# Kernel optimization log

Measured on AMD Instinct MI355X. Metric: run time of the kernel, lower is better.

The kernel has to match this reference:

```python
import jax, jax.numpy as jnp
import numpy as np

DIM = 128
NUM_LAYERS = 2
FF_MULT = 4
RADIUS = 0.2
K = 8
B, N, L = 8, 2048, 4096
NEG = -1e30


def setup_inputs() -> dict:
    key = jax.random.key(0)
    ks = jax.random.split(key, 12)
    C = DIM
    s = 1.0 / np.sqrt(C)
    w = lambda k, shape, sc: jax.random.normal(k, shape, dtype=jnp.float32) * sc
    inp = {
        "q_xyz": jax.random.uniform(ks[0], (B, N, 3), dtype=jnp.float32),
        "q_feat": jax.random.normal(ks[1], (B, N, C), dtype=jnp.float32),
        "kv_xyz": jax.random.uniform(ks[2], (B, L, 3), dtype=jnp.float32),
        "kv_feat": jax.random.normal(ks[3], (B, L, C), dtype=jnp.float32),
        "kv_pad": jnp.zeros((B, L), dtype=bool),
        # PointTransformerConv params (stacked over layers)
        "W_lin": w(ks[4], (NUM_LAYERS, C, C), s),   # value projection (with bias)
        "b_lin": jnp.zeros((NUM_LAYERS, C), jnp.float32),
        "W_src": w(ks[5], (NUM_LAYERS, C, C), s),   # lin_src, no bias
        "W_dst": w(ks[6], (NUM_LAYERS, C, C), s),   # lin_dst, no bias
        "W_attn": w(ks[7], (NUM_LAYERS, C, C), s),  # attn_nn = Linear+ReLU
        "b_attn": jnp.zeros((NUM_LAYERS, C), jnp.float32),
        "ln1_g": jnp.ones((NUM_LAYERS, C), jnp.float32),
        "ln1_b": jnp.zeros((NUM_LAYERS, C), jnp.float32),
        "W_ff1": w(ks[8], (NUM_LAYERS, C, FF_MULT * C), s),
        "b_ff1": jnp.zeros((NUM_LAYERS, FF_MULT * C), jnp.float32),
        "W_ff2": w(ks[9], (NUM_LAYERS, FF_MULT * C, C), 1.0 / np.sqrt(FF_MULT * C)),
        "b_ff2": jnp.zeros((NUM_LAYERS, C), jnp.float32),
        "ln2_g": jnp.ones((NUM_LAYERS, C), jnp.float32),
        "ln2_b": jnp.zeros((NUM_LAYERS, C), jnp.float32),
    }
    return inp


def _layernorm(x, g, b):
    mu = x.mean(-1, keepdims=True)
    var = ((x - mu) ** 2).mean(-1, keepdims=True)
    return (x - mu) * jax.lax.rsqrt(var + 1e-5) * g + b


def _gather(feats, idx):
    # feats: [B, L, C], idx: [B, N, K] -> [B, N, K, C]
    b, n, k = idx.shape
    g = jnp.take_along_axis(feats, idx.reshape(b, n * k)[:, :, None], axis=1)
    return g.reshape(b, n, k, feats.shape[-1])


def _forward(q_xyz, q_feat, kv_xyz, kv_feat, kv_pad,
             W_lin, b_lin, W_src, W_dst, W_attn, b_attn,
             ln1_g, ln1_b, W_ff1, b_ff1, W_ff2, b_ff2, ln2_g, ln2_b):
    # radius neighbor search (per-batch, fixed K neighbors with validity mask)
    d2 = jnp.sum((q_xyz[:, :, None, :] - kv_xyz[:, None, :, :]) ** 2, axis=-1)  # [B,N,L]
    valid_pair = (d2 <= RADIUS * RADIUS) & (~kv_pad)[:, None, :]
    negd = jnp.where(valid_pair, -d2, NEG)
    negv, idx = jax.lax.top_k(negd, K)          # [B,N,K] nearest-in-ball
    evalid = negv > 0.5 * NEG                   # edge validity mask [B,N,K]

    out = q_feat
    for i in range(NUM_LAYERS):
        # PointTransformerConv, pos_nn = ZeroPos => delta = 0
        aj = _gather(kv_feat @ W_src[i], idx)                    # [B,N,K,C]
        vj = _gather(kv_feat @ W_lin[i] + b_lin[i], idx)         # [B,N,K,C]
        ai = out @ W_dst[i]                                      # [B,N,C]
        logits = jax.nn.relu((ai[:, :, None, :] - aj) @ W_attn[i] + b_attn[i])
        logits = jnp.where(evalid[..., None], logits, NEG)
        m = logits.max(axis=2, keepdims=True)
        e = jnp.exp(logits - m) * evalid[..., None]
        attn = e / jnp.maximum(e.sum(axis=2, keepdims=True), 1e-9)  # per-channel softmax over neighbors
        upd = jnp.sum(attn * vj, axis=2)                         # [B,N,C] scatter-add over edges
        out = _layernorm(out + upd, ln1_g[i], ln1_b[i])
        h = jax.nn.gelu(out @ W_ff1[i] + b_ff1[i], approximate=False)
        out = _layernorm(out + h @ W_ff2[i] + b_ff2[i], ln2_g[i], ln2_b[i])
    return out


def reference(q_xyz, q_feat, kv_xyz, kv_feat, kv_pad,
              W_lin, b_lin, W_src, W_dst, W_attn, b_attn,
              ln1_g, ln1_b, W_ff1, b_ff1, W_ff2, b_ff2, ln2_g, ln2_b):
    return _forward(q_xyz, q_feat, kv_xyz, kv_feat, kv_pad,
                    W_lin, b_lin, W_src, W_dst, W_attn, b_attn,
                    ln1_g, ln1_b, W_ff1, b_ff1, W_ff2, b_ff2, ln2_g, ln2_b)
```

## Files before the change

kernel.cpp:

```cpp
#include <hip/hip_runtime.h>
#include <hip/hip_bf16.h>
#include <math.h>

#define DIM 128
#define BB 8
#define NN 2048
#define LL 4096
#define KK 8

typedef __hip_bfloat16 bf16;
typedef unsigned long long ull;
typedef __attribute__((ext_vector_type(8))) short short8;
typedef __attribute__((ext_vector_type(4))) float float4v;

__device__ __forceinline__ float toF(float x){ return x; }
__device__ __forceinline__ float toF(bf16 x){ return __bfloat162float(x); }
__device__ __forceinline__ void st(float* p, float v){ *p = v; }
__device__ __forceinline__ void st(bf16*  p, float v){ *p = __float2bfloat16(v); }
__device__ __forceinline__ unsigned short f2bf(float f){
  union { bf16 b; unsigned short u; } cv; cv.b = __float2bfloat16(f); return cv.u;
}

__device__ __forceinline__ float gelu_exact(float x){
  return 0.5f * x * (1.0f + erff(x * 0.70710678118654752f));
}

__device__ __forceinline__ float waveSum64(float v){
  #pragma unroll
  for (int o = 32; o > 0; o >>= 1) v += __shfl_xor(v, o, 64);
  return v;
}
__device__ __forceinline__ float quadSum16(float v){
  #pragma unroll
  for (int o = 8; o > 0; o >>= 1) v += __shfl_xor(v, o, 64);
  return v;
}

__device__ __forceinline__ void topk_insert_u(ull (&m)[KK], ull key){
  m[KK-1] = key;
  #pragma unroll
  for (int t = KK-1; t > 0; --t){
    if (m[t] < m[t-1]){ ull tmp = m[t]; m[t] = m[t-1]; m[t-1] = tmp; }
  }
}

#define NC3 125
__global__ __launch_bounds__(1024) void knn_bin(const float* __restrict__ kv_xyz,
                                                const float* __restrict__ q_xyz,
                                                float4* __restrict__ bpts,
                                                int* __restrict__ offs ,
                                                int* __restrict__ qsrt )
{
  __shared__ int cnt[NC3];
  __shared__ int off[NC3+1];
  const int b   = blockIdx.x & 7;
  const int role= blockIdx.x >> 3;
  const int tid = threadIdx.x;
  if (tid < NC3) cnt[tid] = 0;
  __syncthreads();
  if (role == 0){
    const float* kvp = kv_xyz + (size_t)b * LL * 3;
    float px[4], py[4], pz[4]; int pc[4];
    #pragma unroll
    for (int i = 0; i < 4; i++){
      const int e = tid + i*1024;
      px[i] = kvp[3*e]; py[i] = kvp[3*e+1]; pz[i] = kvp[3*e+2];
      const int cx = min((int)(px[i]*5.f), 4);
      const int cy = min((int)(py[i]*5.f), 4);
      const int cz = min((int)(pz[i]*5.f), 4);
      pc[i] = (cz*5 + cy)*5 + cx;
      atomicAdd(&cnt[pc[i]], 1);
    }
    __syncthreads();
    if (tid == 0){
      int acc = 0;
      for (int c = 0; c < NC3; c++){ off[c] = acc; acc += cnt[c]; }
      off[NC3] = acc;
    }
    __syncthreads();
    if (tid < NC3) cnt[tid] = 0;
    __syncthreads();
    float4* dst = bpts + (size_t)b * LL;
    #pragma unroll
    for (int i = 0; i < 4; i++){
      const int e = tid + i*1024;
      const int pos = off[pc[i]] + atomicAdd(&cnt[pc[i]], 1);
      dst[pos] = make_float4(px[i], py[i], pz[i], __int_as_float(e));
    }
    if (tid < NC3 + 1) offs[b*126 + tid] = off[tid];
  } else {
    const float* qp = q_xyz + (size_t)b * NN * 3;
    int pc[2];
    #pragma unroll
    for (int i = 0; i < 2; i++){
      const int e = tid + i*1024;
      const float x = qp[3*e], y = qp[3*e+1], z = qp[3*e+2];
      const int cx = min((int)(x*5.f), 4);
      const int cy = min((int)(y*5.f), 4);
      const int cz = min((int)(z*5.f), 4);
      pc[i] = (cz*5 + cy)*5 + cx;
      atomicAdd(&cnt[pc[i]], 1);
    }
    __syncthreads();
    if (tid == 0){
      int acc = 0;
      for (int c = 0; c < NC3; c++){ off[c] = acc; acc += cnt[c]; }
      off[NC3] = acc;
    }
    __syncthreads();
    if (tid < NC3) cnt[tid] = 0;
    __syncthreads();
    int* dst = qsrt + (size_t)b * NN;
    #pragma unroll
    for (int i = 0; i < 2; i++){
      const int e = tid + i*1024;
      const int pos = off[pc[i]] + atomicAdd(&cnt[pc[i]], 1);
      dst[pos] = e;
    }
  }
}

#define QBLK 8
#define SPL 32
__global__ __launch_bounds__(256) void knn_query(const float* __restrict__ q_xyz,
                                                 const float4* __restrict__ bpts,
                                                 const int* __restrict__ offs,
                                                 const int* __restrict__ qsrt,
                                                 int* __restrict__ idx)
{
  __shared__ ull cd[QBLK*257];
  const int tid  = threadIdx.x;
  const int s    = tid >> 3;
  const int qloc = tid & 7;
  const int b    = blockIdx.y;
  const int qbase = blockIdx.x * QBLK;
  const int qid = qsrt[b*NN + qbase + qloc];
  const size_t qo = ((size_t)b * NN + qid) * 3;
  const float qx = q_xyz[qo], qy = q_xyz[qo+1], qz = q_xyz[qo+2];
  const ull THRKEY = ((ull)0x3D23D70Bu << 32);
  ull kthr = THRKEY;
  ull m[KK];
  #pragma unroll
  for (int k = 0; k < KK; k++) m[k] = ~0ULL;
  const int qcx = min((int)(qx*5.f), 4);
  const int qcy = min((int)(qy*5.f), 4);
  const int qcz = min((int)(qz*5.f), 4);
  const int* ofb = offs + b*126;
  const float4* bp = bpts + (size_t)b * LL;
  const int cx0 = max(qcx-1, 0), cx1 = min(qcx+1, 4);
  for (int cz = max(qcz-1,0); cz <= min(qcz+1,4); cz++){
    for (int cy = max(qcy-1,0); cy <= min(qcy+1,4); cy++){
      const int rowc = (cz*5 + cy)*5;
      const int pstart = ofb[rowc + cx0];
      const int pend   = ofb[rowc + cx1 + 1];
      for (int p = pstart + s; p < pend; p += SPL){
        const float4 pt = bp[p];
        const float dx = qx - pt.x, dy = qy - pt.y, dz = qz - pt.z;
        const float d2 = dx*dx + dy*dy + dz*dz;
        const ull key = ((ull)__float_as_uint(d2) << 32) | (unsigned)__float_as_int(pt.w);
        if (key < kthr){
          topk_insert_u(m, key);
          kthr = (m[KK-1] < THRKEY) ? m[KK-1] : THRKEY;
        }
      }
    }
  }
  #pragma unroll
  for (int k = 0; k < KK; k++) cd[qloc*257 + s*8 + k] = m[k];
  __syncthreads();
  if (tid < 64){
    const int q = tid >> 3, g = tid & 7;
    ull mm[KK];
    #pragma unroll
    for (int k = 0; k < KK; k++) mm[k] = ~0ULL;
    #pragma unroll
    for (int u = 0; u < 4; u++){
      const int sl = g + 8*u;
      #pragma unroll
      for (int k = 0; k < KK; k++){
        const ull key = cd[q*257 + sl*8 + k];
        if (key < mm[KK-1]) topk_insert_u(mm, key);
      }
    }
    #pragma unroll
    for (int k = 0; k < KK; k++) cd[q*257 + g*8 + k] = mm[k];
    if (tid < QBLK){
      ull f[KK];
      #pragma unroll
      for (int k = 0; k < KK; k++) f[k] = ~0ULL;
      for (int j = 0; j < 64; j++){
        const ull key = cd[tid*257 + j];
        if (key < f[KK-1]) topk_insert_u(f, key);
      }
      const int oq = b * NN + qsrt[b*NN + qbase + tid];
      #pragma unroll
      for (int k = 0; k < KK; k++) idx[oq*KK + k] = (int)(unsigned)(f[k] & 0xFFFFFFFFu);
    }
  }
}

__device__ __forceinline__ void packOne(const float* __restrict__ src,
                                        bf16* __restrict__ dst, int idx, int nshift){
  const int k = idx >> nshift;
  const int n = idx & ((1 << nshift) - 1);
  const int N = 1 << nshift;
  st(&dst[((size_t)(k>>3)*N + n)*8 + (k&7)], src[idx]);
}

__global__ __launch_bounds__(256) void prep_weights(const float* __restrict__ Wlin,
                                                    const float* __restrict__ Wff1,
                                                    const float* __restrict__ Wff2,
                                                    const float* __restrict__ Wsrc,
                                                    const float* __restrict__ Wdst,
                                                    const float* __restrict__ Wattn,
                                                    bf16* __restrict__ WlinP,
                                                    bf16* __restrict__ Wff1P,
                                                    bf16* __restrict__ Wff2P,
                                                    bf16* __restrict__ WsaP,
                                                    bf16* __restrict__ WdaP)
{
  __shared__ float row[2][DIM];
  const int bid = blockIdx.x;
  if (bid < 1152){
    int i = bid*256 + threadIdx.x;
    if (i < 32768){
      const int l = i >> 14, r = i & 16383;
      packOne(Wlin + (size_t)l*16384, WlinP + (size_t)l*16384, r, 7);
    } else if (i < 163840){
      i -= 32768;
      const int l = i >> 16, r = i & 65535;
      packOne(Wff1 + (size_t)l*65536, Wff1P + (size_t)l*65536, r, 9);
    } else if (i < 294912){
      i -= 163840;
      const int l = i >> 16, r = i & 65535;
      packOne(Wff2 + (size_t)l*65536, Wff2P + (size_t)l*65536, r, 7);
    }
  } else {
    const int half = threadIdx.x >> 7;
    const int c = threadIdx.x & 127;
    const int tt = (bid - 1152)*2 + half;
    const int r = tt & 127, which = (tt >> 7) & 1, lay = tt >> 8;
    const float* Wx = (which ? Wdst : Wsrc) + (size_t)lay*DIM*DIM;
    const float* Wa = Wattn + (size_t)lay*DIM*DIM;
    row[half][c] = Wx[r*DIM + c];
    __syncthreads();
    float acc = 0.f;
    for (int j = 0; j < DIM; j++) acc = fmaf(row[half][j], Wa[j*DIM + c], acc);
    bf16* dst = (which ? WdaP : WsaP) + (size_t)lay*DIM*DIM;
    st(&dst[((size_t)(r>>3)*DIM + c)*8 + (r&7)], acc);
  }
}

__device__ __forceinline__ void stage_A_f32(const float* __restrict__ A, size_t r0,
                                            int kd, int kc, unsigned short* As, int tid){
  #pragma unroll
  for (int i = 0; i < 8; i++){
    const int f = tid + i*256;
    const int row = f >> 5, c4 = (f & 31) * 4;
    const float4 v = *(const float4*)&A[(r0+row)*kd + kc + c4];
    uint2 u;
    u.x = (unsigned)f2bf(v.x) | ((unsigned)f2bf(v.y) << 16);
    u.y = (unsigned)f2bf(v.z) | ((unsigned)f2bf(v.w) << 16);
    *(uint2*)&As[row*136 + c4] = u;
  }
}
__device__ __forceinline__ void stage_A_bf16(const bf16* __restrict__ A, size_t r0,
                                             int kd, int kc, unsigned short* As, int tid){
  #pragma unroll
  for (int i = 0; i < 8; i++){
    const int f = tid + i*256;
    const int row = f >> 5, c4 = (f & 31) * 4;
    *(uint2*)&As[row*136 + c4] = *(const uint2*)&A[(r0+row)*kd + kc + c4];
  }
}

template<typename TA, int NDIM, bool GELU>
__global__ __launch_bounds__(256) void mfma_single(const TA* __restrict__ A,
                                                   const bf16* __restrict__ Wp,
                                                   const float* __restrict__ bias,
                                                   bf16* __restrict__ Y)
{
  __shared__ __align__(16) unsigned short As[64*136];
  const int tid = threadIdx.x;
  const size_t r0 = (size_t)blockIdx.x * 64;
  const int nblk = blockIdx.y * 128;
  if (sizeof(TA) == 4) stage_A_f32((const float*)A, r0, 128, 0, As, tid);
  else                 stage_A_bf16((const bf16*)A, r0, 128, 0, As, tid);
  __syncthreads();
  const int wid = tid >> 6, ln = tid & 63, qd = ln >> 4, cl = ln & 15;
  float4v acc[8];
  #pragma unroll
  for (int t = 0; t < 8; t++) acc[t] = (float4v){0.f,0.f,0.f,0.f};
  #pragma unroll
  for (int ks = 0; ks < 4; ks++){
    const short8 a = *(const short8*)&As[(wid*16 + cl)*136 + (ks*4 + qd)*8];
    const short8* wb = (const short8*)Wp + (size_t)(ks*4 + qd)*NDIM + nblk + cl;
    #pragma unroll
    for (int t = 0; t < 8; t++){
      const short8 b = wb[t*16];
      acc[t] = __builtin_amdgcn_mfma_f32_16x16x32_bf16(a, b, acc[t], 0, 0, 0);
    }
  }
  #pragma unroll
  for (int t = 0; t < 8; t++){
    const int col = nblk + t*16 + cl;
    const float bv = bias ? bias[col] : 0.f;
    #pragma unroll
    for (int r = 0; r < 4; r++){
      const size_t row = r0 + wid*16 + qd*4 + r;
      float v = acc[t][r] + bv;
      if (GELU) v = gelu_exact(v);
      st(&Y[row*NDIM + col], v);
    }
  }
}

__global__ __launch_bounds__(256) void mfma_dual_qa(const float* __restrict__ kvf,
                                                    const float* __restrict__ featIn,
                                                    const bf16* __restrict__ Wp0,
                                                    const bf16* __restrict__ Wp1,
                                                    const bf16* __restrict__ WpQ,
                                                    const float* __restrict__ bias1,
                                                    bf16* __restrict__ Y0,
                                                    bf16* __restrict__ Y1,
                                                    bf16* __restrict__ Yq)
{
  __shared__ __align__(16) unsigned short As[64*136];
  const int tid = threadIdx.x;
  const int wid = tid >> 6, ln = tid & 63, qd = ln >> 4, cl = ln & 15;
  if (blockIdx.x < 512){
    const size_t r0 = (size_t)blockIdx.x * 64;
    stage_A_f32(kvf, r0, 128, 0, As, tid);
    __syncthreads();
    float4v ac0[8], ac1[8];
    #pragma unroll
    for (int t = 0; t < 8; t++){ ac0[t] = (float4v){0.f,0.f,0.f,0.f}; ac1[t] = (float4v){0.f,0.f,0.f,0.f}; }
    #pragma unroll
    for (int ks = 0; ks < 4; ks++){
      const short8 a = *(const short8*)&As[(wid*16 + cl)*136 + (ks*4 + qd)*8];
      const size_t wo = (size_t)(ks*4 + qd)*DIM + cl;
      const short8* wb0 = (const short8*)Wp0 + wo;
      const short8* wb1 = (const short8*)Wp1 + wo;
      #pragma unroll
      for (int t = 0; t < 8; t++){
        const short8 b0 = wb0[t*16];
        ac0[t] = __builtin_amdgcn_mfma_f32_16x16x32_bf16(a, b0, ac0[t], 0, 0, 0);
        const short8 b1 = wb1[t*16];
        ac1[t] = __builtin_amdgcn_mfma_f32_16x16x32_bf16(a, b1, ac1[t], 0, 0, 0);
      }
    }
    #pragma unroll
    for (int t = 0; t < 8; t++){
      const int col = t*16 + cl;
      const float bv = bias1[col];
      #pragma unroll
      for (int r = 0; r < 4; r++){
        const size_t row = r0 + wid*16 + qd*4 + r;
        st(&Y0[row*DIM + col], ac0[t][r]);
        st(&Y1[row*DIM + col], ac1[t][r] + bv);
      }
    }
  } else {
    const size_t r0 = (size_t)(blockIdx.x - 512) * 64;
    stage_A_f32(featIn, r0, 128, 0, As, tid);
    __syncthreads();
    float4v acc[8];
    #pragma unroll
    for (int t = 0; t < 8; t++) acc[t] = (float4v){0.f,0.f,0.f,0.f};
    #pragma unroll
    for (int ks = 0; ks < 4; ks++){
      const short8 a = *(const short8*)&As[(wid*16 + cl)*136 + (ks*4 + qd)*8];
      const short8* wb = (const short8*)WpQ + (size_t)(ks*4 + qd)*DIM + cl;
      #pragma unroll
      for (int t = 0; t < 8; t++){
        const short8 b = wb[t*16];
        acc[t] = __builtin_amdgcn_mfma_f32_16x16x32_bf16(a, b, acc[t], 0, 0, 0);
      }
    }
    #pragma unroll
    for (int t = 0; t < 8; t++){
      const int col = t*16 + cl;
      #pragma unroll
      for (int r = 0; r < 4; r++){
        const size_t row = r0 + wid*16 + qd*4 + r;
        st(&Yq[row*DIM + col], acc[t][r]);
      }
    }
  }
}

__global__ __launch_bounds__(256) void mfma_ff2ln(const bf16* __restrict__ A,
                                                  const bf16* __restrict__ Wp,
                                                  const float* __restrict__ b2,
                                                  const bf16* __restrict__ resid,
                                                  const float* __restrict__ g,
                                                  const float* __restrict__ bb,
                                                  float* __restrict__ Y)
{
  __shared__ __align__(16) unsigned short As[64*136];
  const int tid = threadIdx.x;
  const size_t r0 = (size_t)blockIdx.x * 64;
  const int wid = tid >> 6, ln = tid & 63, qd = ln >> 4, cl = ln & 15;
  float4v acc[8];
  #pragma unroll
  for (int t = 0; t < 8; t++) acc[t] = (float4v){0.f,0.f,0.f,0.f};
  for (int kc = 0; kc < 512; kc += 128){
    __syncthreads();
    stage_A_bf16(A, r0, 512, kc, As, tid);
    __syncthreads();
    const int k8c = kc >> 3;
    #pragma unroll
    for (int ks = 0; ks < 4; ks++){
      const short8 a = *(const short8*)&As[(wid*16 + cl)*136 + (ks*4 + qd)*8];
      const short8* wb = (const short8*)Wp + (size_t)(k8c + ks*4 + qd)*DIM + cl;
      #pragma unroll
      for (int t = 0; t < 8; t++){
        const short8 b = wb[t*16];
        acc[t] = __builtin_amdgcn_mfma_f32_16x16x32_bf16(a, b, acc[t], 0, 0, 0);
      }
    }
  }
  float v[8][4];
  #pragma unroll
  for (int t = 0; t < 8; t++){
    const int col = t*16 + cl;
    const float bv = b2[col];
    #pragma unroll
    for (int r = 0; r < 4; r++){
      const size_t row = r0 + wid*16 + qd*4 + r;
      v[t][r] = acc[t][r] + bv + toF(resid[row*DIM + col]);
    }
  }
  #pragma unroll
  for (int r = 0; r < 4; r++){
    float s = 0.f;
    #pragma unroll
    for (int t = 0; t < 8; t++) s += v[t][r];
    const float mu = quadSum16(s) * (1.f/DIM);
    float q = 0.f;
    #pragma unroll
    for (int t = 0; t < 8; t++){ const float d = v[t][r] - mu; q += d*d; }
    const float inv = rsqrtf(quadSum16(q) * (1.f/DIM) + 1e-5f);
    const size_t row = r0 + wid*16 + qd*4 + r;
    #pragma unroll
    for (int t = 0; t < 8; t++){
      const int col = t*16 + cl;
      Y[row*DIM + col] = (v[t][r] - mu) * inv * g[col] + bb[col];
    }
  }
}

__global__ __launch_bounds__(256) void attn_ln1(const bf16* __restrict__ qA,
                                                const bf16* __restrict__ srcA,
                                                const bf16* __restrict__ linp,
                                                const int* __restrict__ idx,
                                                const int* __restrict__ qsrt,
                                                const float* __restrict__ b_attn,
                                                const float* __restrict__ feat,
                                                const float* __restrict__ g,
                                                const float* __restrict__ bb,
                                                bf16* __restrict__ out1)
{
  const int tid = threadIdx.x;
  const int wv = tid >> 6, ln = tid & 63;
  const int sp = blockIdx.x * 4 + wv;
  const int b = sp >> 11;
  const int q = b * NN + qsrt[b*NN + (sp & 2047)];
  const bf16* sbase = srcA + (size_t)b * LL * DIM;
  const bf16* vbase = linp + (size_t)b * LL * DIM;
  const int c0 = ln, c1 = ln + 64;
  const float qa0 = toF(qA[(size_t)q*DIM + c0]) + b_attn[c0];
  const float qa1 = toF(qA[(size_t)q*DIM + c1]) + b_attn[c1];
  int ids[KK]; float l0[KK], l1[KK];
  float m0 = -1e30f, m1 = -1e30f;
  #pragma unroll
  for (int k = 0; k < KK; k++){
    const int id = idx[q*KK + k]; ids[k] = id;
    if (id >= 0){
      const float s0 = toF(sbase[(size_t)id*DIM + c0]);
      const float s1 = toF(sbase[(size_t)id*DIM + c1]);
      l0[k] = fmaxf(qa0 - s0, 0.f); m0 = fmaxf(m0, l0[k]);
      l1[k] = fmaxf(qa1 - s1, 0.f); m1 = fmaxf(m1, l1[k]);
    } else { l0[k] = 0.f; l1[k] = 0.f; }
  }
  float sum0 = 0.f, sum1 = 0.f, upd0 = 0.f, upd1 = 0.f;
  #pragma unroll
  for (int k = 0; k < KK; k++) if (ids[k] >= 0){
    const float e0 = expf(l0[k] - m0); l0[k] = e0; sum0 += e0;
    const float e1 = expf(l1[k] - m1); l1[k] = e1; sum1 += e1;
  }
  if (sum0 > 0.f){
    const float i0 = 1.f / sum0, i1 = 1.f / sum1;
    #pragma unroll
    for (int k = 0; k < KK; k++) if (ids[k] >= 0){
      upd0 = fmaf(l0[k]*i0, toF(vbase[(size_t)ids[k]*DIM + c0]), upd0);
      upd1 = fmaf(l1[k]*i1, toF(vbase[(size_t)ids[k]*DIM + c1]), upd1);
    }
  }
  const float x0 = feat[(size_t)q*DIM + c0] + upd0;
  const float x1 = feat[(size_t)q*DIM + c1] + upd1;
  const float mu = waveSum64(x0 + x1) * (1.f/DIM);
  const float d0 = x0 - mu, d1 = x1 - mu;
  const float var = waveSum64(d0*d0 + d1*d1) * (1.f/DIM);
  const float inv = rsqrtf(var + 1e-5f);
  st(&out1[(size_t)q*DIM + c0], d0 * inv * g[c0] + bb[c0]);
  st(&out1[(size_t)q*DIM + c1], d1 * inv * g[c1] + bb[c1]);
}

extern "C" void kernel_launch(void* const* d_in, const int* in_sizes, int n_in,
                              void* d_out, int out_size, void* d_ws, size_t ws_size,
                              hipStream_t stream)
{
  const float* q_xyz  = (const float*)d_in[0];
  const float* q_feat = (const float*)d_in[1];
  const float* kv_xyz = (const float*)d_in[2];
  const float* kv_feat= (const float*)d_in[3];
  const float* W_lin  = (const float*)d_in[5];
  const float* b_lin  = (const float*)d_in[6];
  const float* W_src  = (const float*)d_in[7];
  const float* W_dst  = (const float*)d_in[8];
  const float* W_attn = (const float*)d_in[9];
  const float* b_attn = (const float*)d_in[10];
  const float* ln1_g  = (const float*)d_in[11];
  const float* ln1_b  = (const float*)d_in[12];
  const float* W_ff1  = (const float*)d_in[13];
  const float* b_ff1  = (const float*)d_in[14];
  const float* W_ff2  = (const float*)d_in[15];
  const float* b_ff2  = (const float*)d_in[16];
  const float* ln2_g  = (const float*)d_in[17];
  const float* ln2_b  = (const float*)d_in[18];
  float* out = (float*)d_out;

  const int MQ  = BB * NN;
  const int MKV = BB * LL;

  char* p = (char*)d_ws;
  int*    idxb  = (int*)p;    p += (size_t)MQ * KK * 4;
  float4* bpts  = (float4*)p; p += (size_t)BB * LL * 16;
  int*    boffs = (int*)p;    p += (size_t)BB * 126 * 4;
  int*    qsrt  = (int*)p;    p += (size_t)BB * NN * 4;
  bf16*  WsaP  = (bf16*)p;  p += (size_t)2 * DIM * DIM * 2;
  bf16*  WdaP  = (bf16*)p;  p += (size_t)2 * DIM * DIM * 2;
  bf16*  WlinP = (bf16*)p;  p += (size_t)2 * DIM * DIM * 2;
  bf16*  Wff1P = (bf16*)p;  p += (size_t)2 * DIM * 4*DIM * 2;
  bf16*  Wff2P = (bf16*)p;  p += (size_t)2 * 4*DIM * DIM * 2;
  float* feat  = (float*)p; p += (size_t)MQ * DIM * 4;
  bf16*  out1  = (bf16*)p;  p += (size_t)MQ * DIM * 2;
  bf16*  srcA  = (bf16*)p;  p += (size_t)MKV * DIM * 2;
  bf16*  linp  = (bf16*)p;  p += (size_t)MKV * DIM * 2;
  bf16*  qA    = (bf16*)p;  p += (size_t)MQ * DIM * 2;
  bf16*  hbuf  = srcA;

  knn_bin<<<16, 1024, 0, stream>>>(kv_xyz, q_xyz, bpts, boffs, qsrt);
  knn_query<<<dim3(NN/QBLK, BB), 256, 0, stream>>>(q_xyz, bpts, boffs, qsrt, idxb);
  prep_weights<<<1152 + 256, 256, 0, stream>>>(W_lin, W_ff1, W_ff2, W_src, W_dst,
                                               W_attn, WlinP, Wff1P, Wff2P, WsaP, WdaP);

  for (int i = 0; i < 2; i++){
    const size_t w128 = (size_t)i * DIM * DIM;
    const size_t w512 = (size_t)i * DIM * 4*DIM;
    const float* featIn = (i == 0) ? q_feat : feat;

    mfma_dual_qa<<<MKV/64 + MQ/64, 256, 0, stream>>>(kv_feat, featIn,
        WsaP + w128, WlinP + w128, WdaP + w128, b_lin + i*DIM, srcA, linp, qA);
    attn_ln1<<<MQ/4, 256, 0, stream>>>(qA, srcA, linp, idxb, qsrt, b_attn + i*DIM,
                                       featIn, ln1_g + i*DIM, ln1_b + i*DIM, out1);
    mfma_single<bf16, 512, true><<<dim3(MQ/64, 4), 256, 0, stream>>>(
        out1, Wff1P + w512, b_ff1 + i*4*DIM, hbuf);
    float* ydst = (i == 1) ? out : feat;
    mfma_ff2ln<<<MQ/64, 256, 0, stream>>>(hbuf, Wff2P + w512, b_ff2 + i*DIM, out1,
                                          ln2_g + i*DIM, ln2_b + i*DIM, ydst);
  }
}
```

Before: 297.4 us.

## Merge binning and weight prep kernels, remap kNN lanes, vectorize attention loads

```diff
diff --git a/kernel.cpp b/kernel.cpp
--- a/kernel.cpp
+++ b/kernel.cpp
@@ -20,6 +20,13 @@
 __device__ __forceinline__ unsigned short f2bf(float f){
   union { bf16 b; unsigned short u; } cv; cv.b = __float2bfloat16(f); return cv.u;
 }
+__device__ __forceinline__ float2 ld2bf(const bf16* p){
+  const unsigned u = *(const unsigned*)p;
+  return make_float2(__uint_as_float(u << 16), __uint_as_float(u & 0xFFFF0000u));
+}
+__device__ __forceinline__ void st2bf(bf16* p, float a, float b){
+  *(unsigned*)p = (unsigned)f2bf(a) | ((unsigned)f2bf(b) << 16);
+}
 
 __device__ __forceinline__ float gelu_exact(float x){
   return 0.5f * x * (1.0f + erff(x * 0.70710678118654752f));
@@ -45,78 +52,128 @@
 }
 
 #define NC3 125
-__global__ __launch_bounds__(1024) void knn_bin(const float* __restrict__ kv_xyz,
-                                                const float* __restrict__ q_xyz,
-                                                float4* __restrict__ bpts,
-                                                int* __restrict__ offs ,
-                                                int* __restrict__ qsrt )
+__device__ __forceinline__ void packOne(const float* __restrict__ src,
+                                        bf16* __restrict__ dst, int idx, int nshift){
+  const int k = idx >> nshift;
+  const int n = idx & ((1 << nshift) - 1);
+  const int N = 1 << nshift;
+  st(&dst[((size_t)(k>>3)*N + n)*8 + (k&7)], src[idx]);
+}
+
+__global__ __launch_bounds__(1024) void setup_all(const float* __restrict__ kv_xyz,
+                                                  const float* __restrict__ q_xyz,
+                                                  float4* __restrict__ bpts,
+                                                  int* __restrict__ offs,
+                                                  int* __restrict__ qsrt,
+                                                  const float* __restrict__ Wlin,
+                                                  const float* __restrict__ Wff1,
+                                                  const float* __restrict__ Wff2,
+                                                  const float* __restrict__ Wsrc,
+                                                  const float* __restrict__ Wdst,
+                                                  const float* __restrict__ Wattn,
+                                                  bf16* __restrict__ WlinP,
+                                                  bf16* __restrict__ Wff1P,
+                                                  bf16* __restrict__ Wff2P,
+                                                  bf16* __restrict__ WsaP,
+                                                  bf16* __restrict__ WdaP)
 {
   __shared__ int cnt[NC3];
   __shared__ int off[NC3+1];
-  const int b   = blockIdx.x & 7;
-  const int role= blockIdx.x >> 3;
+  __shared__ float row[8][DIM];
+  const int bid = blockIdx.x;
   const int tid = threadIdx.x;
-  if (tid < NC3) cnt[tid] = 0;
-  __syncthreads();
-  if (role == 0){
-    const float* kvp = kv_xyz + (size_t)b * LL * 3;
-    float px[4], py[4], pz[4]; int pc[4];
-    #pragma unroll
-    for (int i = 0; i < 4; i++){
-      const int e = tid + i*1024;
-      px[i] = kvp[3*e]; py[i] = kvp[3*e+1]; pz[i] = kvp[3*e+2];
-      const int cx = min((int)(px[i]*5.f), 4);
-      const int cy = min((int)(py[i]*5.f), 4);
-      const int cz = min((int)(pz[i]*5.f), 4);
-      pc[i] = (cz*5 + cy)*5 + cx;
-      atomicAdd(&cnt[pc[i]], 1);
-    }
-    __syncthreads();
-    if (tid == 0){
-      int acc = 0;
-      for (int c = 0; c < NC3; c++){ off[c] = acc; acc += cnt[c]; }
-      off[NC3] = acc;
-    }
-    __syncthreads();
+  if (bid < 16){
+    const int b   = bid & 7;
+    const int role= bid >> 3;
     if (tid < NC3) cnt[tid] = 0;
     __syncthreads();
-    float4* dst = bpts + (size_t)b * LL;
-    #pragma unroll
-    for (int i = 0; i < 4; i++){
-      const int e = tid + i*1024;
-      const int pos = off[pc[i]] + atomicAdd(&cnt[pc[i]], 1);
-      dst[pos] = make_float4(px[i], py[i], pz[i], __int_as_float(e));
-    }
-    if (tid < NC3 + 1) offs[b*126 + tid] = off[tid];
+    if (role == 0){
+      const float* kvp = kv_xyz + (size_t)b * LL * 3;
+      float px[4], py[4], pz[4]; int pc[4];
+      #pragma unroll
+      for (int i = 0; i < 4; i++){
+        const int e = tid + i*1024;
+        px[i] = kvp[3*e]; py[i] = kvp[3*e+1]; pz[i] = kvp[3*e+2];
+        const int cx = min((int)(px[i]*5.f), 4);
+        const int cy = min((int)(py[i]*5.f), 4);
+        const int cz = min((int)(pz[i]*5.f), 4);
+        pc[i] = (cz*5 + cy)*5 + cx;
+        atomicAdd(&cnt[pc[i]], 1);
+      }
+      __syncthreads();
+      if (tid == 0){
+        int acc = 0;
+        for (int c = 0; c < NC3; c++){ off[c] = acc; acc += cnt[c]; }
+        off[NC3] = acc;
+      }
+      __syncthreads();
+      if (tid < NC3) cnt[tid] = 0;
+      __syncthreads();
+      float4* dst = bpts + (size_t)b * LL;
+      #pragma unroll
+      for (int i = 0; i < 4; i++){
+        const int e = tid + i*1024;
+        const int pos = off[pc[i]] + atomicAdd(&cnt[pc[i]], 1);
+        dst[pos] = make_float4(px[i], py[i], pz[i], __int_as_float(e));
+      }
+      if (tid < NC3 + 1) offs[b*126 + tid] = off[tid];
+    } else {
+      const float* qp = q_xyz + (size_t)b * NN * 3;
+      int pc[2];
+      #pragma unroll
+      for (int i = 0; i < 2; i++){
+        const int e = tid + i*1024;
+        const float x = qp[3*e], y = qp[3*e+1], z = qp[3*e+2];
+        const int cx = min((int)(x*5.f), 4);
+        const int cy = min((int)(y*5.f), 4);
+        const int cz = min((int)(z*5.f), 4);
+        pc[i] = (cz*5 + cy)*5 + cx;
+        atomicAdd(&cnt[pc[i]], 1);
+      }
+      __syncthreads();
+      if (tid == 0){
+        int acc = 0;
+        for (int c = 0; c < NC3; c++){ off[c] = acc; acc += cnt[c]; }
+        off[NC3] = acc;
+      }
+      __syncthreads();
+      if (tid < NC3) cnt[tid] = 0;
+      __syncthreads();
+      int* dst = qsrt + (size_t)b * NN;
+      #pragma unroll
+      for (int i = 0; i < 2; i++){
+        const int e = tid + i*1024;
+        const int pos = off[pc[i]] + atomicAdd(&cnt[pc[i]], 1);
+        dst[pos] = e;
+      }
+    }
+  } else if (bid < 304){
+    int i = (bid - 16)*1024 + tid;
+    if (i < 32768){
+      const int l = i >> 14, r = i & 16383;
+      packOne(Wlin + (size_t)l*16384, WlinP + (size_t)l*16384, r, 7);
+    } else if (i < 163840){
+      i -= 32768;
+      const int l = i >> 16, r = i & 65535;
+      packOne(Wff1 + (size_t)l*65536, Wff1P + (size_t)l*65536, r, 9);
+    } else {
+      i -= 163840;
+      const int l = i >> 16, r = i & 65535;
+      packOne(Wff2 + (size_t)l*65536, Wff2P + (size_t)l*65536, r, 7);
+    }
   } else {
-    const float* qp = q_xyz + (size_t)b * NN * 3;
-    int pc[2];
-    #pragma unroll
-    for (int i = 0; i < 2; i++){
-      const int e = tid + i*1024;
-      const float x = qp[3*e], y = qp[3*e+1], z = qp[3*e+2];
-      const int cx = min((int)(x*5.f), 4);
-      const int cy = min((int)(y*5.f), 4);
-      const int cz = min((int)(z*5.f), 4);
-      pc[i] = (cz*5 + cy)*5 + cx;
-      atomicAdd(&cnt[pc[i]], 1);
-    }
+    const int grp = tid >> 7;
+    const int c = tid & 127;
+    const int tt = (bid - 304)*8 + grp;
+    const int r = tt & 127, which = (tt >> 7) & 1, lay = tt >> 8;
+    const float* Wx = (which ? Wdst : Wsrc) + (size_t)lay*DIM*DIM;
+    const float* Wa = Wattn + (size_t)lay*DIM*DIM;
+    row[grp][c] = Wx[r*DIM + c];
     __syncthreads();
-    if (tid == 0){
-      int acc = 0;
-      for (int c = 0; c < NC3; c++){ off[c] = acc; acc += cnt[c]; }
-      off[NC3] = acc;
-    }
-    __syncthreads();
-    if (tid < NC3) cnt[tid] = 0;
-    __syncthreads();
-    int* dst = qsrt + (size_t)b * NN;
-    #pragma unroll
-    for (int i = 0; i < 2; i++){
-      const int e = tid + i*1024;
-      const int pos = off[pc[i]] + atomicAdd(&cnt[pc[i]], 1);
-      dst[pos] = e;
-    }
+    float acc = 0.f;
+    for (int j = 0; j < DIM; j++) acc = fmaf(row[grp][j], Wa[j*DIM + c], acc);
+    bf16* dst = (which ? WdaP : WsaP) + (size_t)lay*DIM*DIM;
+    st(&dst[((size_t)(r>>3)*DIM + c)*8 + (r&7)], acc);
   }
 }
 
@@ -130,8 +187,8 @@
 {
   __shared__ ull cd[QBLK*257];
   const int tid  = threadIdx.x;
-  const int s    = tid >> 3;
-  const int qloc = tid & 7;
+  const int s    = tid & 31;
+  const int qloc = tid >> 5;
   const int b    = blockIdx.y;
   const int qbase = blockIdx.x * QBLK;
   const int qid = qsrt[b*NN + qbase + qloc];
@@ -151,22 +208,30 @@
   for (int cz = max(qcz-1,0); cz <= min(qcz+1,4); cz++){
     for (int cy = max(qcy-1,0); cy <= min(qcy+1,4); cy++){
       const int rowc = (cz*5 + cy)*5;
-      const int pstart = ofb[rowc + cx0];
-      const int pend   = ofb[rowc + cx1 + 1];
-      for (int p = pstart + s; p < pend; p += SPL){
-        const float4 pt = bp[p];
-        const float dx = qx - pt.x, dy = qy - pt.y, dz = qz - pt.z;
-        const float d2 = dx*dx + dy*dy + dz*dz;
-        const ull key = ((ull)__float_as_uint(d2) << 32) | (unsigned)__float_as_int(pt.w);
-        if (key < kthr){
-          topk_insert_u(m, key);
-          kthr = (m[KK-1] < THRKEY) ? m[KK-1] : THRKEY;
+      const int pend = ofb[rowc + cx1 + 1];
+      int p = ofb[rowc + cx0] + s;
+      if (p < pend){
+        float4 pt = bp[p];
+        while (true){
+          const int pn = p + SPL;
+          const bool hn = pn < pend;
+          float4 nx;
+          if (hn) nx = bp[pn];
+          const float dx = qx - pt.x, dy = qy - pt.y, dz = qz - pt.z;
+          const float d2 = dx*dx + dy*dy + dz*dz;
+          const ull key = ((ull)__float_as_uint(d2) << 32) | (unsigned)__float_as_int(pt.w);
+          if (key < kthr){
+            topk_insert_u(m, key);
+            kthr = (m[KK-1] < THRKEY) ? m[KK-1] : THRKEY;
+          }
+          if (!hn) break;
+          pt = nx; p = pn;
         }
       }
     }
   }
   #pragma unroll
-  for (int k = 0; k < KK; k++) cd[qloc*257 + s*8 + k] = m[k];
+  for (int k = 0; k < KK; k++) cd[qloc*257 + k*32 + s] = m[k];
   __syncthreads();
   if (tid < 64){
     const int q = tid >> 3, g = tid & 7;
@@ -178,76 +243,26 @@
       const int sl = g + 8*u;
       #pragma unroll
       for (int k = 0; k < KK; k++){
-        const ull key = cd[q*257 + sl*8 + k];
+        const ull key = cd[q*257 + k*32 + sl];
         if (key < mm[KK-1]) topk_insert_u(mm, key);
       }
     }
     #pragma unroll
-    for (int k = 0; k < KK; k++) cd[q*257 + g*8 + k] = mm[k];
+    for (int k = 0; k < KK; k++) cd[q*257 + k*32 + g] = mm[k];
     if (tid < QBLK){
       ull f[KK];
       #pragma unroll
       for (int k = 0; k < KK; k++) f[k] = ~0ULL;
-      for (int j = 0; j < 64; j++){
-        const ull key = cd[tid*257 + j];
-        if (key < f[KK-1]) topk_insert_u(f, key);
-      }
+      #pragma unroll
+      for (int k = 0; k < 8; k++)
+        for (int g2 = 0; g2 < 8; g2++){
+          const ull key = cd[tid*257 + k*32 + g2];
+          if (key < f[KK-1]) topk_insert_u(f, key);
+        }
       const int oq = b * NN + qsrt[b*NN + qbase + tid];
       #pragma unroll
       for (int k = 0; k < KK; k++) idx[oq*KK + k] = (int)(unsigned)(f[k] & 0xFFFFFFFFu);
     }
-  }
-}
-
-__device__ __forceinline__ void packOne(const float* __restrict__ src,
-                                        bf16* __restrict__ dst, int idx, int nshift){
-  const int k = idx >> nshift;
-  const int n = idx & ((1 << nshift) - 1);
-  const int N = 1 << nshift;
-  st(&dst[((size_t)(k>>3)*N + n)*8 + (k&7)], src[idx]);
-}
-
-__global__ __launch_bounds__(256) void prep_weights(const float* __restrict__ Wlin,
-                                                    const float* __restrict__ Wff1,
-                                                    const float* __restrict__ Wff2,
-                                                    const float* __restrict__ Wsrc,
-                                                    const float* __restrict__ Wdst,
-                                                    const float* __restrict__ Wattn,
-                                                    bf16* __restrict__ WlinP,
-                                                    bf16* __restrict__ Wff1P,
-                                                    bf16* __restrict__ Wff2P,
-                                                    bf16* __restrict__ WsaP,
-                                                    bf16* __restrict__ WdaP)
-{
-  __shared__ float row[2][DIM];
-  const int bid = blockIdx.x;
-  if (bid < 1152){
-    int i = bid*256 + threadIdx.x;
-    if (i < 32768){
-      const int l = i >> 14, r = i & 16383;
-      packOne(Wlin + (size_t)l*16384, WlinP + (size_t)l*16384, r, 7);
-    } else if (i < 163840){
-      i -= 32768;
-      const int l = i >> 16, r = i & 65535;
-      packOne(Wff1 + (size_t)l*65536, Wff1P + (size_t)l*65536, r, 9);
-    } else if (i < 294912){
-      i -= 163840;
-      const int l = i >> 16, r = i & 65535;
-      packOne(Wff2 + (size_t)l*65536, Wff2P + (size_t)l*65536, r, 7);
-    }
-  } else {
-    const int half = threadIdx.x >> 7;
-    const int c = threadIdx.x & 127;
-    const int tt = (bid - 1152)*2 + half;
-    const int r = tt & 127, which = (tt >> 7) & 1, lay = tt >> 8;
-    const float* Wx = (which ? Wdst : Wsrc) + (size_t)lay*DIM*DIM;
-    const float* Wa = Wattn + (size_t)lay*DIM*DIM;
-    row[half][c] = Wx[r*DIM + c];
-    __syncthreads();
-    float acc = 0.f;
-    for (int j = 0; j < DIM; j++) acc = fmaf(row[half][j], Wa[j*DIM + c], acc);
-    bf16* dst = (which ? WdaP : WsaP) + (size_t)lay*DIM*DIM;
-    st(&dst[((size_t)(r>>3)*DIM + c)*8 + (r&7)], acc);
   }
 }
 
@@ -468,19 +483,19 @@
   const int q = b * NN + qsrt[b*NN + (sp & 2047)];
   const bf16* sbase = srcA + (size_t)b * LL * DIM;
   const bf16* vbase = linp + (size_t)b * LL * DIM;
-  const int c0 = ln, c1 = ln + 64;
-  const float qa0 = toF(qA[(size_t)q*DIM + c0]) + b_attn[c0];
-  const float qa1 = toF(qA[(size_t)q*DIM + c1]) + b_attn[c1];
+  const int c0 = 2*ln;
+  const float2 ba = *(const float2*)&b_attn[c0];
+  const float2 qa2 = ld2bf(&qA[(size_t)q*DIM + c0]);
+  const float qa0 = qa2.x + ba.x, qa1 = qa2.y + ba.y;
   int ids[KK]; float l0[KK], l1[KK];
   float m0 = -1e30f, m1 = -1e30f;
   #pragma unroll
   for (int k = 0; k < KK; k++){
     const int id = idx[q*KK + k]; ids[k] = id;
     if (id >= 0){
-      const float s0 = toF(sbase[(size_t)id*DIM + c0]);
-      const float s1 = toF(sbase[(size_t)id*DIM + c1]);
-      l0[k] = fmaxf(qa0 - s0, 0.f); m0 = fmaxf(m0, l0[k]);
-      l1[k] = fmaxf(qa1 - s1, 0.f); m1 = fmaxf(m1, l1[k]);
+      const float2 s2 = ld2bf(&sbase[(size_t)id*DIM + c0]);
+      l0[k] = fmaxf(qa0 - s2.x, 0.f); m0 = fmaxf(m0, l0[k]);
+      l1[k] = fmaxf(qa1 - s2.y, 0.f); m1 = fmaxf(m1, l1[k]);
     } else { l0[k] = 0.f; l1[k] = 0.f; }
   }
   float sum0 = 0.f, sum1 = 0.f, upd0 = 0.f, upd1 = 0.f;
@@ -493,18 +508,21 @@
     const float i0 = 1.f / sum0, i1 = 1.f / sum1;
     #pragma unroll
     for (int k = 0; k < KK; k++) if (ids[k] >= 0){
-      upd0 = fmaf(l0[k]*i0, toF(vbase[(size_t)ids[k]*DIM + c0]), upd0);
-      upd1 = fmaf(l1[k]*i1, toF(vbase[(size_t)ids[k]*DIM + c1]), upd1);
-    }
-  }
-  const float x0 = feat[(size_t)q*DIM + c0] + upd0;
-  const float x1 = feat[(size_t)q*DIM + c1] + upd1;
+      const float2 v2 = ld2bf(&vbase[(size_t)ids[k]*DIM + c0]);
+      upd0 = fmaf(l0[k]*i0, v2.x, upd0);
+      upd1 = fmaf(l1[k]*i1, v2.y, upd1);
+    }
+  }
+  const float2 f2 = *(const float2*)&feat[(size_t)q*DIM + c0];
+  const float x0 = f2.x + upd0;
+  const float x1 = f2.y + upd1;
   const float mu = waveSum64(x0 + x1) * (1.f/DIM);
   const float d0 = x0 - mu, d1 = x1 - mu;
   const float var = waveSum64(d0*d0 + d1*d1) * (1.f/DIM);
   const float inv = rsqrtf(var + 1e-5f);
-  st(&out1[(size_t)q*DIM + c0], d0 * inv * g[c0] + bb[c0]);
-  st(&out1[(size_t)q*DIM + c1], d1 * inv * g[c1] + bb[c1]);
+  const float2 gg = *(const float2*)&g[c0];
+  const float2 bbv = *(const float2*)&bb[c0];
+  st2bf(&out1[(size_t)q*DIM + c0], d0 * inv * gg.x + bbv.x, d1 * inv * gg.y + bbv.y);
 }
 
 extern "C" void kernel_launch(void* const* d_in, const int* in_sizes, int n_in,
@@ -551,10 +569,10 @@
   bf16*  qA    = (bf16*)p;  p += (size_t)MQ * DIM * 2;
   bf16*  hbuf  = srcA;
 
-  knn_bin<<<16, 1024, 0, stream>>>(kv_xyz, q_xyz, bpts, boffs, qsrt);
+  setup_all<<<368, 1024, 0, stream>>>(kv_xyz, q_xyz, bpts, boffs, qsrt,
+                                      W_lin, W_ff1, W_ff2, W_src, W_dst, W_attn,
+                                      WlinP, Wff1P, Wff2P, WsaP, WdaP);
   knn_query<<<dim3(NN/QBLK, BB), 256, 0, stream>>>(q_xyz, bpts, boffs, qsrt, idxb);
-  prep_weights<<<1152 + 256, 256, 0, stream>>>(W_lin, W_ff1, W_ff2, W_src, W_dst,
-                                               W_attn, WlinP, Wff1P, Wff2P, WsaP, WdaP);
 
   for (int i = 0; i < 2; i++){
     const size_t w128 = (size_t)i * DIM * DIM;
```

New measurement: 288.4 us. -3.0%, faster.
